# Performance work log

Measured on AMD Instinct MI355X. Metric: run time of the kernel, lower is better.

The kernel has to match this reference:

```python
import jax, jax.numpy as jnp
import numpy as np

NUM_HEADS = 16

def _rope_tables(seq_len, head_dim, dtype):
    inv_freq = 1.0 / (10000.0 ** (jnp.arange(0, head_dim, 2, dtype=jnp.float32) / head_dim))
    t = jnp.arange(seq_len, dtype=jnp.float32)
    freqs = jnp.einsum('i,j->ij', t, inv_freq)          # [S, hd/2]
    emb = jnp.concatenate([freqs, freqs], axis=-1)      # [S, hd]
    return jnp.cos(emb).astype(dtype), jnp.sin(emb).astype(dtype)

def _rotate_half(x):
    x1, x2 = jnp.split(x, 2, axis=-1)
    return jnp.concatenate([-x2, x1], axis=-1)

def _apply_rope(x, cos, sin):
    # x: [B, H, S, hd]; cos/sin: [S, hd]
    return x * cos + _rotate_half(x) * sin

def setup_inputs() -> dict:
    key = jax.random.key(0)
    ks = jax.random.split(key, 9)
    S, B, E = 2048, 2, 1024
    sc_w = 1.0 / np.sqrt(E)
    inp = {
        'query': jax.random.normal(ks[0], (S, B, E), jnp.float32),
        'wq': jax.random.normal(ks[1], (E, E), jnp.float32) * sc_w,
        'bq': jax.random.normal(ks[2], (E,), jnp.float32) * 0.02,
        'wk': jax.random.normal(ks[3], (E, E), jnp.float32) * sc_w,
        'bk': jax.random.normal(ks[4], (E,), jnp.float32) * 0.02,
        'wv': jax.random.normal(ks[5], (E, E), jnp.float32) * sc_w,
        'bv': jax.random.normal(ks[6], (E,), jnp.float32) * 0.02,
        'wo': jax.random.normal(ks[7], (E, E), jnp.float32) * sc_w,
        'bo': jax.random.normal(ks[8], (E,), jnp.float32) * 0.02,
    }
    return inp

def reference(query, wq, bq, wk, bk, wv, bv, wo, bo):
    S, B, E = query.shape
    H = NUM_HEADS
    hd = E // H
    # QKV projections (torch Linear: x @ W^T + b). self_attention => k,v from query.
    q = jnp.einsum('sbe,fe->sbf', query, wq) + bq
    k = jnp.einsum('sbe,fe->sbf', query, wk) + bk
    v = jnp.einsum('sbe,fe->sbf', query, wv) + bv
    # [S, B, E] -> [B, H, S, hd]
    def to_bhsd(x):
        return x.reshape(S, B, H, hd).transpose(1, 2, 0, 3)
    q, k, v = to_bhsd(q), to_bhsd(k), to_bhsd(v)
    cos, sin = _rope_tables(S, hd, query.dtype)
    q = _apply_rope(q, cos, sin)
    k = _apply_rope(k, cos, sin)
    # scaled dot-product attention (no mask, no dropout)
    scale = 1.0 / jnp.sqrt(jnp.asarray(hd, query.dtype))
    scores = jnp.einsum('bhqd,bhkd->bhqk', q, k) * scale
    probs = jax.nn.softmax(scores, axis=-1)
    attn = jnp.einsum('bhqk,bhkd->bhqd', probs, v)
    # [B, H, S, hd] -> [S, B, E]
    attn = attn.transpose(2, 0, 1, 3).reshape(S, B, E)
    out = jnp.einsum('sbe,fe->sbf', attn, wo) + bo
    return out
```

## Files before the change

### kernel.cpp

```cpp
#include <hip/hip_runtime.h>
#include <stdint.h>

#define S_LEN 2048
#define BATCH 2
#define EMB   1024
#define NHEAD 16
#define HDIM  64

typedef __bf16 bf8   __attribute__((ext_vector_type(8)));
typedef float  f32x4 __attribute__((ext_vector_type(4)));
typedef float  f32x16 __attribute__((ext_vector_type(16)));

__device__ __forceinline__ unsigned short f2bf(float f) {
    unsigned u = __builtin_bit_cast(unsigned, f);
    u += 0x7fffu + ((u >> 16) & 1u);
    return (unsigned short)(u >> 16);
}
__device__ __forceinline__ float bf2f(unsigned short h) {
    unsigned u = ((unsigned)h) << 16;
    return __builtin_bit_cast(float, u);
}
__device__ __forceinline__ float fexp2(float x) { return __builtin_amdgcn_exp2f(x); }
__device__ __forceinline__ float f3max(float a, float b, float c) { return fmaxf(fmaxf(a, b), c); }

__device__ __forceinline__ void gl_lds16(const unsigned short* g, unsigned short* l) {
    __builtin_amdgcn_global_load_lds(
        (__attribute__((address_space(1))) void*)(void*)g,
        (__attribute__((address_space(3))) void*)(void*)l, 16, 0, 0);
}

__global__ void k_tables(float* __restrict__ cosT, float* __restrict__ sinT) {
    int idx = blockIdx.x * 256 + threadIdx.x;
    int s = idx >> 6, d = idx & 63, j = d & 31;
    float inv = exp2f(-13.28771237954945f * ((float)j * (1.0f / 32.0f)));
    float ang = (float)s * inv;
    cosT[idx] = cosf(ang);
    sinT[idx] = sinf(ang);
}

__global__ void k_cast_x(const float* __restrict__ x, unsigned short* __restrict__ xb) {
    int id = blockIdx.x * 256 + threadIdx.x;
    int b = id >> 19, rem = id & 524287;
    int s = rem >> 8, e4 = (rem & 255) << 2;
    float4 v = *(const float4*)&x[((size_t)(s * BATCH + b)) * EMB + e4];
    ushort4 o;
    o.x = f2bf(v.x); o.y = f2bf(v.y); o.z = f2bf(v.z); o.w = f2bf(v.w);
    *(ushort4*)&xb[((size_t)(b * S_LEN + s)) * EMB + e4] = o;
}

__global__ void k_castW(const float* __restrict__ w0, const float* __restrict__ w1,
                        const float* __restrict__ w2, const float* __restrict__ w3,
                        unsigned short* __restrict__ o0, unsigned short* __restrict__ o1,
                        unsigned short* __restrict__ o2, unsigned short* __restrict__ o3) {
    int id = blockIdx.x * 256 + threadIdx.x;
    int seg = id >> 18, r = id & 262143;
    const float* s = seg == 0 ? w0 : seg == 1 ? w1 : seg == 2 ? w2 : w3;
    unsigned short* o = seg == 0 ? o0 : seg == 1 ? o1 : seg == 2 ? o2 : o3;
    float4 v = *(const float4*)&s[(size_t)r * 4];
    ushort4 u;
    u.x = f2bf(v.x); u.y = f2bf(v.y); u.z = f2bf(v.z); u.w = f2bf(v.w);
    *(ushort4*)&o[(size_t)r * 4] = u;
}

__global__ void __launch_bounds__(256) k_gemmQKV(
    const unsigned short* __restrict__ A,
    const unsigned short* __restrict__ Wq, const unsigned short* __restrict__ Wk,
    const unsigned short* __restrict__ Wv,
    const float* __restrict__ bqp, const float* __restrict__ bkp, const float* __restrict__ bvp,
    unsigned short* __restrict__ qout, unsigned short* __restrict__ kout,
    unsigned short* __restrict__ vout,
    const float* __restrict__ cosT, const float* __restrict__ sinT)
{
    __shared__ __align__(16) unsigned short As[128 * 32];
    __shared__ __align__(16) unsigned short Bs[128 * 32];
    const int z = blockIdx.z;
    const unsigned short* B = z == 0 ? Wq : z == 1 ? Wk : Wv;
    const float* bias = z == 0 ? bqp : z == 1 ? bkp : bvp;
    const int tid  = threadIdx.x;
    const int lane = tid & 63;
    const int wid  = tid >> 6;
    const int wm = wid >> 1, wn = wid & 1;
    const int l15 = lane & 15, lh = lane >> 4;
    const int tm0 = blockIdx.y * 128, tn0 = blockIdx.x * 128;
    const int K = 1024;

    f32x4 acc[4][4] = {};

    for (int k0 = 0; k0 < K; k0 += 32) {
        __syncthreads();
#pragma unroll
        for (int rnd = 0; rnd < 2; ++rnd) {
            int cbase = wid * 64 + rnd * 256;
            int c = cbase + lane;
            int row = c >> 2, co = (c & 3) * 8;
            gl_lds16(A + (size_t)(tm0 + row) * K + k0 + co, &As[cbase * 8]);
            gl_lds16(B + (size_t)(tn0 + row) * K + k0 + co, &Bs[cbase * 8]);
        }
        __syncthreads();
        bf8 a[4], b[4];
#pragma unroll
        for (int i = 0; i < 4; ++i) {
            a[i] = *(const bf8*)&As[(wm * 64 + i * 16 + l15) * 32 + lh * 8];
            b[i] = *(const bf8*)&Bs[(wn * 64 + i * 16 + l15) * 32 + lh * 8];
        }
#pragma unroll
        for (int i = 0; i < 4; ++i)
#pragma unroll
            for (int j = 0; j < 4; ++j)
                acc[i][j] = __builtin_amdgcn_mfma_f32_16x16x32_bf16(a[i], b[j], acc[i][j], 0, 0, 0);
    }

    if (z < 2) {
        unsigned short* C = z ? kout : qout;
        const float f = z ? 1.0f : 0.125f * 1.44269504089f;
#pragma unroll
        for (int i = 0; i < 4; ++i) {
            const int rowb = tm0 + wm * 64 + i * 16 + lh * 4;
#pragma unroll
            for (int j = 0; j < 2; ++j) {
                const int col = tn0 + wn * 64 + j * 16 + l15;
                const int d = j * 16 + l15;
#pragma unroll
                for (int r = 0; r < 4; ++r) {
                    int m = rowb + r;
                    int sq = m & (S_LEN - 1);
                    float x1 = acc[i][j][r]     + bias[col];
                    float x2 = acc[i][j + 2][r] + bias[col + 32];
                    float c  = cosT[sq * 64 + d] * f;
                    float sn = sinT[sq * 64 + d] * f;
                    C[(size_t)m * EMB + col]      = f2bf(x1 * c - x2 * sn);
                    C[(size_t)m * EMB + col + 32] = f2bf(x2 * c + x1 * sn);
                }
            }
        }
    } else {
#pragma unroll
        for (int i = 0; i < 4; ++i) {
            const int rowb = tm0 + wm * 64 + i * 16 + lh * 4;
#pragma unroll
            for (int j = 0; j < 4; ++j) {
                const int col = tn0 + wn * 64 + j * 16 + l15;
                float bv = bias[col];
#pragma unroll
                for (int r = 0; r < 4; ++r)
                    vout[(size_t)col * 4096 + rowb + r] = f2bf(acc[i][j][r] + bv);
            }
        }
    }
}

__global__ void __launch_bounds__(256) k_attn8(
    const unsigned short* __restrict__ qb,
    const unsigned short* __restrict__ kb,
    const unsigned short* __restrict__ vT,
    float* __restrict__ po0, float* __restrict__ po1,
    float* __restrict__ ml)
{
    __shared__ __align__(16) unsigned short Sm[24576];
    __shared__ float bl[4][32];
    const int tid = threadIdx.x, lane = tid & 63, wid = tid >> 6;
    const int l31 = lane & 31, hi = lane >> 5;
    const int bh = blockIdx.y;
    const int b = bh >> 4, h = bh & 15;
    const int z = blockIdx.z;
    const int kv0 = z << 10;
    const int q0 = blockIdx.x * 128 + wid * 32;
    float* __restrict__ po = z ? po1 : po0;
    float* __restrict__ mlz = ml + (size_t)z * (32 * 2048 * 2);

    const unsigned short* qrow = qb + ((size_t)(b * S_LEN + q0 + l31)) * EMB + h * HDIM + hi * 8;
    bf8 qf[4];
#pragma unroll
    for (int c = 0; c < 4; ++c) qf[c] = *(const bf8*)(qrow + c * 16);

    const int mz = l31 & 7;
    const int koA0 = l31 * 128 + (((0 * 2 + hi) ^ mz) << 4);
    const int koA1 = l31 * 128 + (((1 * 2 + hi) ^ mz) << 4);
    const int koA2 = l31 * 128 + (((2 * 2 + hi) ^ mz) << 4);
    const int koA3 = l31 * 128 + (((3 * 2 + hi) ^ mz) << 4);
    const char* ldsc = (const char*)Sm;

    const int srow = lane >> 3, sp = lane & 7;
    const int r0 = wid * 16 + srow,     p0s = sp ^ (r0 & 7);
    const int r1 = wid * 16 + 8 + srow, p1s = sp ^ (r1 & 7);
    const int kgo0 = (r0 * EMB + p0s * 8) * 2, kgo1 = (r1 * EMB + p1s * 8) * 2;
    const int vgo0 = (r0 * (S_LEN * BATCH) + p0s * 8) * 2, vgo1 = (r1 * (S_LEN * BATCH) + p1s * 8) * 2;

    const unsigned short* kS = kb + ((size_t)(b * S_LEN + kv0)) * EMB + h * HDIM;
    const unsigned short* vS = vT + ((size_t)h * HDIM) * (S_LEN * BATCH) + b * S_LEN + kv0;

#define STAGE8(DBUF) do { \
    gl_lds16((const unsigned short*)((const char*)kS + kgo0), Sm + (DBUF) * 4096 + wid * 1024); \
    gl_lds16((const unsigned short*)((const char*)vS + vgo0), Sm + 12288 + (DBUF) * 4096 + wid * 1024); \
    gl_lds16((const unsigned short*)((const char*)kS + kgo1), Sm + (DBUF) * 4096 + wid * 1024 + 512); \
    gl_lds16((const unsigned short*)((const char*)vS + vgo1), Sm + 12288 + (DBUF) * 4096 + wid * 1024 + 512); \
    kS += 64 * EMB; vS += 64; } while (0)

    auto pack2 = [](float lo, float hh) -> unsigned {
        unsigned short a  = __builtin_bit_cast(unsigned short, (__bf16)lo);
        unsigned short bb = __builtin_bit_cast(unsigned short, (__bf16)hh);
        return ((unsigned)bb << 16) | a;
    };

    float m_run = 0.f, l_run = 0.f;
    f32x16 oacc0 = {}, oacc1 = {};
    const f32x16 Z16 = {};

    STAGE8(0);
    STAGE8(1);

#define ABODY(BUF, DOSTG, LASTW) do { \
    if (LASTW) asm volatile("s_waitcnt vmcnt(0)" ::: "memory"); \
    else       asm volatile("s_waitcnt vmcnt(4)" ::: "memory"); \
    __builtin_amdgcn_s_barrier(); \
    if (DOSTG) STAGE8(((BUF) + 2) % 3); \
    bf8 ka0 = *(const bf8*)(ldsc + koA0 + (BUF) * 8192); \
    bf8 ka1 = *(const bf8*)(ldsc + koA1 + (BUF) * 8192); \
    bf8 ka2 = *(const bf8*)(ldsc + koA2 + (BUF) * 8192); \
    bf8 ka3 = *(const bf8*)(ldsc + koA3 + (BUF) * 8192); \
    bf8 kb0 = *(const bf8*)(ldsc + koA0 + (BUF) * 8192 + 4096); \
    bf8 kb1 = *(const bf8*)(ldsc + koA1 + (BUF) * 8192 + 4096); \
    bf8 kb2 = *(const bf8*)(ldsc + koA2 + (BUF) * 8192 + 4096); \
    bf8 kb3 = *(const bf8*)(ldsc + koA3 + (BUF) * 8192 + 4096); \
    __builtin_amdgcn_s_setprio(1); \
    f32x16 stA = __builtin_amdgcn_mfma_f32_32x32x16_bf16(ka0, qf[0], Z16, 0, 0, 0); \
    f32x16 stB = __builtin_amdgcn_mfma_f32_32x32x16_bf16(kb0, qf[0], Z16, 0, 0, 0); \
    stA = __builtin_amdgcn_mfma_f32_32x32x16_bf16(ka1, qf[1], stA, 0, 0, 0); \
    stB = __builtin_amdgcn_mfma_f32_32x32x16_bf16(kb1, qf[1], stB, 0, 0, 0); \
    stA = __builtin_amdgcn_mfma_f32_32x32x16_bf16(ka2, qf[2], stA, 0, 0, 0); \
    stB = __builtin_amdgcn_mfma_f32_32x32x16_bf16(kb2, qf[2], stB, 0, 0, 0); \
    stA = __builtin_amdgcn_mfma_f32_32x32x16_bf16(ka3, qf[3], stA, 0, 0, 0); \
    stB = __builtin_amdgcn_mfma_f32_32x32x16_bf16(kb3, qf[3], stB, 0, 0, 0); \
    __builtin_amdgcn_s_setprio(0); \
    float g0 = f3max(f3max(stA[0], stA[1], stA[2]),  f3max(stA[3], stA[4], stA[5]),  f3max(stA[6], stA[7], stA[8])); \
    float g1 = f3max(f3max(stA[9], stA[10], stA[11]), f3max(stA[12], stA[13], stA[14]), fmaxf(stA[15], stB[0])); \
    float g2 = f3max(f3max(stB[1], stB[2], stB[3]),  f3max(stB[4], stB[5], stB[6]),  f3max(stB[7], stB[8], stB[9])); \
    float g3 = f3max(f3max(stB[10], stB[11], stB[12]), f3max(stB[13], stB[14], stB[15]), fmaxf(g0, g1)); \
    float pmax = f3max(g2, g3, g0); \
    pmax = fmaxf(pmax, __shfl_xor(pmax, 32)); \
    if (!__all(pmax - m_run <= 11.54f)) { \
        float mnew = fmaxf(m_run, pmax); \
        float corr = fexp2(m_run - mnew); \
        l_run *= corr; m_run = mnew; \
        if (hi == 0) bl[wid][l31] = corr; \
        asm volatile("s_waitcnt lgkmcnt(0)" ::: "memory"); \
        _Pragma("unroll") for (int r = 0; r < 16; ++r) { \
            float c2 = bl[wid][(r & 3) + 8 * (r >> 2) + 4 * hi]; \
            oacc0[r] *= c2; oacc1[r] *= c2; } \
    } \
    float pA[16], pB[16]; \
    _Pragma("unroll") for (int r = 0; r < 16; ++r) pA[r] = fexp2(stA[r] - m_run); \
    _Pragma("unroll") for (int r = 0; r < 16; ++r) pB[r] = fexp2(stB[r] - m_run); \
    float sA = (((pA[0] + pA[1]) + (pA[2] + pA[3])) + ((pA[4] + pA[5]) + (pA[6] + pA[7]))) \
             + (((pA[8] + pA[9]) + (pA[10] + pA[11])) + ((pA[12] + pA[13]) + (pA[14] + pA[15]))); \
    float sB = (((pB[0] + pB[1]) + (pB[2] + pB[3])) + ((pB[4] + pB[5]) + (pB[6] + pB[7]))) \
             + (((pB[8] + pB[9]) + (pB[10] + pB[11])) + ((pB[12] + pB[13]) + (pB[14] + pB[15]))); \
    float psum = sA + sB; \
    psum += __shfl_xor(psum, 32); \
    l_run += psum; \
    unsigned a0w = pack2(pA[0], pA[1]),  a1w = pack2(pA[2], pA[3]); \
    unsigned a2w = pack2(pA[4], pA[5]),  a3w = pack2(pA[6], pA[7]); \
    unsigned a4w = pack2(pA[8], pA[9]),  a5w = pack2(pA[10], pA[11]); \
    unsigned a6w = pack2(pA[12], pA[13]), a7w = pack2(pA[14], pA[15]); \
    unsigned rA_ = (unsigned)__shfl_xor((int)(hi ? a0w : a2w), 32); \
    unsigned rB_ = (unsigned)__shfl_xor((int)(hi ? a1w : a3w), 32); \
    unsigned rC_ = (unsigned)__shfl_xor((int)(hi ? a4w : a6w), 32); \
    unsigned rD_ = (unsigned)__shfl_xor((int)(hi ? a5w : a7w), 32); \
    uint4 uA0 = hi ? uint4{rA_, rB_, a2w, a3w} : uint4{a0w, a1w, rA_, rB_}; \
    uint4 uA1 = hi ? uint4{rC_, rD_, a6w, a7w} : uint4{a4w, a5w, rC_, rD_}; \
    bf8 pf0A = __builtin_bit_cast(bf8, uA0); \
    bf8 pf1A = __builtin_bit_cast(bf8, uA1); \
    unsigned b0w = pack2(pB[0], pB[1]),  b1w = pack2(pB[2], pB[3]); \
    unsigned b2w = pack2(pB[4], pB[5]),  b3w = pack2(pB[6], pB[7]); \
    unsigned b4w = pack2(pB[8], pB[9]),  b5w = pack2(pB[10], pB[11]); \
    unsigned b6w = pack2(pB[12], pB[13]), b7w = pack2(pB[14], pB[15]); \
    unsigned rE_ = (unsigned)__shfl_xor((int)(hi ? b0w : b2w), 32); \
    unsigned rF_ = (unsigned)__shfl_xor((int)(hi ? b1w : b3w), 32); \
    unsigned rG_ = (unsigned)__shfl_xor((int)(hi ? b4w : b6w), 32); \
    unsigned rH_ = (unsigned)__shfl_xor((int)(hi ? b5w : b7w), 32); \
    uint4 uB0 = hi ? uint4{rE_, rF_, b2w, b3w} : uint4{b0w, b1w, rE_, rF_}; \
    uint4 uB1 = hi ? uint4{rG_, rH_, b6w, b7w} : uint4{b4w, b5w, rG_, rH_}; \
    bf8 pf0B = __builtin_bit_cast(bf8, uB0); \
    bf8 pf1B = __builtin_bit_cast(bf8, uB1); \
    bf8 va0 = *(const bf8*)(ldsc + koA0 + 24576 + (BUF) * 8192); \
    bf8 va1 = *(const bf8*)(ldsc + koA1 + 24576 + (BUF) * 8192); \
    bf8 va2 = *(const bf8*)(ldsc + koA2 + 24576 + (BUF) * 8192); \
    bf8 va3 = *(const bf8*)(ldsc + koA3 + 24576 + (BUF) * 8192); \
    bf8 vb0 = *(const bf8*)(ldsc + koA0 + 24576 + (BUF) * 8192 + 4096); \
    bf8 vb1 = *(const bf8*)(ldsc + koA1 + 24576 + (BUF) * 8192 + 4096); \
    bf8 vb2 = *(const bf8*)(ldsc + koA2 + 24576 + (BUF) * 8192 + 4096); \
    bf8 vb3 = *(const bf8*)(ldsc + koA3 + 24576 + (BUF) * 8192 + 4096); \
    __builtin_amdgcn_s_setprio(1); \
    oacc0 = __builtin_amdgcn_mfma_f32_32x32x16_bf16(pf0A, va0, oacc0, 0, 0, 0); \
    oacc1 = __builtin_amdgcn_mfma_f32_32x32x16_bf16(pf0A, vb0, oacc1, 0, 0, 0); \
    oacc0 = __builtin_amdgcn_mfma_f32_32x32x16_bf16(pf1A, va1, oacc0, 0, 0, 0); \
    oacc1 = __builtin_amdgcn_mfma_f32_32x32x16_bf16(pf1A, vb1, oacc1, 0, 0, 0); \
    oacc0 = __builtin_amdgcn_mfma_f32_32x32x16_bf16(pf0B, va2, oacc0, 0, 0, 0); \
    oacc1 = __builtin_amdgcn_mfma_f32_32x32x16_bf16(pf0B, vb2, oacc1, 0, 0, 0); \
    oacc0 = __builtin_amdgcn_mfma_f32_32x32x16_bf16(pf1B, va3, oacc0, 0, 0, 0); \
    oacc1 = __builtin_amdgcn_mfma_f32_32x32x16_bf16(pf1B, vb3, oacc1, 0, 0, 0); \
    __builtin_amdgcn_s_setprio(0); \
} while (0)

    for (int t3 = 0; t3 < 5; ++t3) {
        ABODY(0, true, false);
        ABODY(1, true, false);
        ABODY(2, (t3 < 4), false);
    }
    ABODY(0, false, true);

#undef ABODY
#undef STAGE8

#pragma unroll
    for (int r = 0; r < 16; ++r) {
        int q = (r & 3) + 8 * (r >> 2) + 4 * hi;
        size_t base = ((size_t)bh * 2048 + q0 + q) * 64 + l31;
        po[base]      = oacc0[r];
        po[base + 32] = oacc1[r];
    }
    if (hi == 0) {
        size_t mi = ((size_t)bh * 2048 + q0 + l31) * 2;
        mlz[mi]     = m_run;
        mlz[mi + 1] = l_run;
    }
}

__global__ void k_comb(const float* __restrict__ po0, const float* __restrict__ po1,
                       const float* __restrict__ ml, unsigned short* __restrict__ ob)
{
    int id = blockIdx.x * 256 + threadIdx.x;
    int d4 = (id & 15) * 4;
    int q  = (id >> 4) & 2047;
    int bh = id >> 15;
    int b = bh >> 4, h = bh & 15;
    size_t mi = ((size_t)bh * 2048 + q) * 2;
    float m0 = ml[mi], l0 = ml[mi + 1];
    float m1 = ml[mi + (size_t)32 * 2048 * 2], l1 = ml[mi + (size_t)32 * 2048 * 2 + 1];
    float m = fmaxf(m0, m1);
    float w0 = fexp2(m0 - m), w1 = fexp2(m1 - m);
    float inv = 1.0f / (l0 * w0 + l1 * w1);
    size_t pi = ((size_t)bh * 2048 + q) * 64 + d4;
    float4 a = *(const float4*)&po0[pi];
    float4 c = *(const float4*)&po1[pi];
    ushort4 o;
    o.x = f2bf((a.x * w0 + c.x * w1) * inv);
    o.y = f2bf((a.y * w0 + c.y * w1) * inv);
    o.z = f2bf((a.z * w0 + c.z * w1) * inv);
    o.w = f2bf((a.w * w0 + c.w * w1) * inv);
    *(ushort4*)&ob[((size_t)(b * S_LEN + q)) * EMB + h * HDIM + d4] = o;
}

template<int EPI, typename OutT>
__global__ void __launch_bounds__(256) k_gemm(
    const unsigned short* __restrict__ A,
    const unsigned short* __restrict__ B,
    const float* __restrict__ bias,
    OutT* __restrict__ C,
    int M, int N, int K)
{
    __shared__ __align__(16) unsigned short As[128 * 32];
    __shared__ __align__(16) unsigned short Bs[128 * 32];
    const int tid  = threadIdx.x;
    const int lane = tid & 63;
    const int wid  = tid >> 6;
    const int wm = wid >> 1, wn = wid & 1;
    const int l15 = lane & 15, lh = lane >> 4;
    const int tm0 = blockIdx.y * 128, tn0 = blockIdx.x * 128;

    f32x4 acc[4][4] = {};

    for (int k0 = 0; k0 < K; k0 += 32) {
        __syncthreads();
#pragma unroll
        for (int rnd = 0; rnd < 2; ++rnd) {
            int cbase = wid * 64 + rnd * 256;
            int c = cbase + lane;
            int row = c >> 2, co = (c & 3) * 8;
            gl_lds16(A + (size_t)(tm0 + row) * K + k0 + co, &As[cbase * 8]);
            gl_lds16(B + (size_t)(tn0 + row) * K + k0 + co, &Bs[cbase * 8]);
        }
        __syncthreads();
        bf8 a[4], b[4];
#pragma unroll
        for (int i = 0; i < 4; ++i) {
            a[i] = *(const bf8*)&As[(wm * 64 + i * 16 + l15) * 32 + lh * 8];
            b[i] = *(const bf8*)&Bs[(wn * 64 + i * 16 + l15) * 32 + lh * 8];
        }
#pragma unroll
        for (int i = 0; i < 4; ++i)
#pragma unroll
            for (int j = 0; j < 4; ++j)
                acc[i][j] = __builtin_amdgcn_mfma_f32_16x16x32_bf16(a[i], b[j], acc[i][j], 0, 0, 0);
    }

#pragma unroll
    for (int i = 0; i < 4; ++i) {
        const int rowb = tm0 + wm * 64 + i * 16 + lh * 4;
#pragma unroll
        for (int j = 0; j < 4; ++j) {
            const int col = tn0 + wn * 64 + j * 16 + l15;
#pragma unroll
            for (int r = 0; r < 4; ++r) {
                float v = acc[i][j][r];
                int row = rowb + r;
                if (EPI == 0) {
                    v += bias[col];
                    C[(size_t)row * N + col] = (OutT)f2bf(v);
                } else {
                    v += bias[col];
                    int bb = row >> 11, ss = row & 2047;
                    ((float*)C)[(size_t)(ss * BATCH + bb) * N + col] = v;
                }
            }
        }
    }
}

extern "C" void kernel_launch(void* const* d_in, const int* in_sizes, int n_in,
                              void* d_out, int out_size, void* d_ws, size_t ws_size,
                              hipStream_t stream)
{
    (void)in_sizes; (void)n_in; (void)out_size; (void)ws_size;
    const float* query = (const float*)d_in[0];
    const float* wq = (const float*)d_in[1];
    const float* bq = (const float*)d_in[2];
    const float* wk = (const float*)d_in[3];
    const float* bk = (const float*)d_in[4];
    const float* wv = (const float*)d_in[5];
    const float* bv = (const float*)d_in[6];
    const float* wo = (const float*)d_in[7];
    const float* bo = (const float*)d_in[8];

    char* ws = (char*)d_ws;
    float*          cosT = (float*)(ws + 0);
    float*          sinT = (float*)(ws + (512 << 10));
    float*          ml   = (float*)(ws + 0);
    unsigned short* xb   = (unsigned short*)(ws + (1  << 20));
    float*          po0  = (float*)(ws + (1  << 20));
    unsigned short* wqb  = (unsigned short*)(ws + (9  << 20));
    unsigned short* wkb  = (unsigned short*)(ws + (11 << 20));
    unsigned short* wvb  = (unsigned short*)(ws + (13 << 20));
    unsigned short* qb   = (unsigned short*)(ws + (17 << 20));
    unsigned short* ob   = qb;
    unsigned short* kb   = (unsigned short*)(ws + (25 << 20));
    unsigned short* vT   = (unsigned short*)(ws + (33 << 20));
    float*          po1  = (float*)(ws + (41 << 20));
    unsigned short* wob  = (unsigned short*)(ws + (57 << 20));

    k_tables<<<512, 256, 0, stream>>>(cosT, sinT);
    k_cast_x<<<4096, 256, 0, stream>>>(query, xb);
    k_castW<<<4096, 256, 0, stream>>>(wq, wk, wv, wo, wqb, wkb, wvb, wob);

    dim3 gq(EMB / 128, (S_LEN * BATCH) / 128, 3);
    k_gemmQKV<<<gq, 256, 0, stream>>>(xb, wqb, wkb, wvb, bq, bk, bv,
                                      qb, kb, vT, cosT, sinT);

    dim3 g3(S_LEN / 128, BATCH * NHEAD, 2);
    k_attn8<<<g3, 256, 0, stream>>>(qb, kb, vT, po0, po1, ml);
    k_comb<<<4096, 256, 0, stream>>>(po0, po1, ml, ob);

    dim3 g1(EMB / 128, (S_LEN * BATCH) / 128);
    k_gemm<1, float><<<g1, 256, 0, stream>>>(ob, wob, bo, (float*)d_out, 4096, 1024, 1024);
}
```

Baseline: 168.0 us.

## Drop split-KV attention and fuse the three prep kernels into one launch

The attention kernel now sweeps the full KV length in one block instead of two KV halves. It normalizes by the running sum in its epilogue and writes bf16 output directly, so the fp32 partial buffers and the separate combine kernel go away. The table, activation-cast and weight-cast kernels are merged into a single launch that dispatches on block index. This saves launches and the partial-output traffic, but halves the attention grid, which lowers parallelism (512 blocks instead of 1024) and doubles each block's serial loop length.

```diff
diff --git a/kernel.cpp b/kernel.cpp
--- a/kernel.cpp
+++ b/kernel.cpp
@@ -29,37 +29,40 @@
         (__attribute__((address_space(3))) void*)(void*)l, 16, 0, 0);
 }
 
-__global__ void k_tables(float* __restrict__ cosT, float* __restrict__ sinT) {
-    int idx = blockIdx.x * 256 + threadIdx.x;
-    int s = idx >> 6, d = idx & 63, j = d & 31;
-    float inv = exp2f(-13.28771237954945f * ((float)j * (1.0f / 32.0f)));
-    float ang = (float)s * inv;
-    cosT[idx] = cosf(ang);
-    sinT[idx] = sinf(ang);
-}
-
-__global__ void k_cast_x(const float* __restrict__ x, unsigned short* __restrict__ xb) {
-    int id = blockIdx.x * 256 + threadIdx.x;
-    int b = id >> 19, rem = id & 524287;
-    int s = rem >> 8, e4 = (rem & 255) << 2;
-    float4 v = *(const float4*)&x[((size_t)(s * BATCH + b)) * EMB + e4];
-    ushort4 o;
-    o.x = f2bf(v.x); o.y = f2bf(v.y); o.z = f2bf(v.z); o.w = f2bf(v.w);
-    *(ushort4*)&xb[((size_t)(b * S_LEN + s)) * EMB + e4] = o;
-}
-
-__global__ void k_castW(const float* __restrict__ w0, const float* __restrict__ w1,
-                        const float* __restrict__ w2, const float* __restrict__ w3,
-                        unsigned short* __restrict__ o0, unsigned short* __restrict__ o1,
-                        unsigned short* __restrict__ o2, unsigned short* __restrict__ o3) {
-    int id = blockIdx.x * 256 + threadIdx.x;
-    int seg = id >> 18, r = id & 262143;
-    const float* s = seg == 0 ? w0 : seg == 1 ? w1 : seg == 2 ? w2 : w3;
-    unsigned short* o = seg == 0 ? o0 : seg == 1 ? o1 : seg == 2 ? o2 : o3;
-    float4 v = *(const float4*)&s[(size_t)r * 4];
-    ushort4 u;
-    u.x = f2bf(v.x); u.y = f2bf(v.y); u.z = f2bf(v.z); u.w = f2bf(v.w);
-    *(ushort4*)&o[(size_t)r * 4] = u;
+__global__ void k_prep(const float* __restrict__ x,
+                       const float* __restrict__ w0, const float* __restrict__ w1,
+                       const float* __restrict__ w2, const float* __restrict__ w3,
+                       float* __restrict__ cosT, float* __restrict__ sinT,
+                       unsigned short* __restrict__ xb,
+                       unsigned short* __restrict__ o0, unsigned short* __restrict__ o1,
+                       unsigned short* __restrict__ o2, unsigned short* __restrict__ o3)
+{
+    int bid = blockIdx.x;
+    if (bid < 512) {
+        int idx = bid * 256 + threadIdx.x;
+        int s = idx >> 6, d = idx & 63, j = d & 31;
+        float inv = exp2f(-13.28771237954945f * ((float)j * (1.0f / 32.0f)));
+        float ang = (float)s * inv;
+        cosT[idx] = cosf(ang);
+        sinT[idx] = sinf(ang);
+    } else if (bid < 4608) {
+        int id = (bid - 512) * 256 + threadIdx.x;
+        int b = id >> 19, rem = id & 524287;
+        int s = rem >> 8, e4 = (rem & 255) << 2;
+        float4 v = *(const float4*)&x[((size_t)(s * BATCH + b)) * EMB + e4];
+        ushort4 o;
+        o.x = f2bf(v.x); o.y = f2bf(v.y); o.z = f2bf(v.z); o.w = f2bf(v.w);
+        *(ushort4*)&xb[((size_t)(b * S_LEN + s)) * EMB + e4] = o;
+    } else {
+        int id = (bid - 4608) * 256 + threadIdx.x;
+        int seg = id >> 18, r = id & 262143;
+        const float* s = seg == 0 ? w0 : seg == 1 ? w1 : seg == 2 ? w2 : w3;
+        unsigned short* o = seg == 0 ? o0 : seg == 1 ? o1 : seg == 2 ? o2 : o3;
+        float4 v = *(const float4*)&s[(size_t)r * 4];
+        ushort4 u;
+        u.x = f2bf(v.x); u.y = f2bf(v.y); u.z = f2bf(v.z); u.w = f2bf(v.w);
+        *(ushort4*)&o[(size_t)r * 4] = u;
+    }
 }
 
 __global__ void __launch_bounds__(256) k_gemmQKV(
@@ -153,8 +156,7 @@
     const unsigned short* __restrict__ qb,
     const unsigned short* __restrict__ kb,
     const unsigned short* __restrict__ vT,
-    float* __restrict__ po0, float* __restrict__ po1,
-    float* __restrict__ ml)
+    unsigned short* __restrict__ ob)
 {
     __shared__ __align__(16) unsigned short Sm[24576];
     __shared__ float bl[4][32];
@@ -162,11 +164,7 @@
     const int l31 = lane & 31, hi = lane >> 5;
     const int bh = blockIdx.y;
     const int b = bh >> 4, h = bh & 15;
-    const int z = blockIdx.z;
-    const int kv0 = z << 10;
     const int q0 = blockIdx.x * 128 + wid * 32;
-    float* __restrict__ po = z ? po1 : po0;
-    float* __restrict__ mlz = ml + (size_t)z * (32 * 2048 * 2);
 
     const unsigned short* qrow = qb + ((size_t)(b * S_LEN + q0 + l31)) * EMB + h * HDIM + hi * 8;
     bf8 qf[4];
@@ -186,8 +184,8 @@
     const int kgo0 = (r0 * EMB + p0s * 8) * 2, kgo1 = (r1 * EMB + p1s * 8) * 2;
     const int vgo0 = (r0 * (S_LEN * BATCH) + p0s * 8) * 2, vgo1 = (r1 * (S_LEN * BATCH) + p1s * 8) * 2;
 
-    const unsigned short* kS = kb + ((size_t)(b * S_LEN + kv0)) * EMB + h * HDIM;
-    const unsigned short* vS = vT + ((size_t)h * HDIM) * (S_LEN * BATCH) + b * S_LEN + kv0;
+    const unsigned short* kS = kb + ((size_t)(b * S_LEN)) * EMB + h * HDIM;
+    const unsigned short* vS = vT + ((size_t)h * HDIM) * (S_LEN * BATCH) + b * S_LEN;
 
 #define STAGE8(DBUF) do { \
     gl_lds16((const unsigned short*)((const char*)kS + kgo0), Sm + (DBUF) * 4096 + wid * 1024); \
@@ -302,53 +300,27 @@
     __builtin_amdgcn_s_setprio(0); \
 } while (0)
 
-    for (int t3 = 0; t3 < 5; ++t3) {
+    for (int t3 = 0; t3 < 10; ++t3) {
         ABODY(0, true, false);
         ABODY(1, true, false);
-        ABODY(2, (t3 < 4), false);
-    }
-    ABODY(0, false, true);
+        ABODY(2, true, false);
+    }
+    ABODY(0, false, false);
+    ABODY(1, false, true);
 
 #undef ABODY
 #undef STAGE8
 
+    if (hi == 0) bl[wid][l31] = l_run;
+    asm volatile("s_waitcnt lgkmcnt(0)" ::: "memory");
 #pragma unroll
     for (int r = 0; r < 16; ++r) {
         int q = (r & 3) + 8 * (r >> 2) + 4 * hi;
-        size_t base = ((size_t)bh * 2048 + q0 + q) * 64 + l31;
-        po[base]      = oacc0[r];
-        po[base + 32] = oacc1[r];
-    }
-    if (hi == 0) {
-        size_t mi = ((size_t)bh * 2048 + q0 + l31) * 2;
-        mlz[mi]     = m_run;
-        mlz[mi + 1] = l_run;
-    }
-}
-
-__global__ void k_comb(const float* __restrict__ po0, const float* __restrict__ po1,
-                       const float* __restrict__ ml, unsigned short* __restrict__ ob)
-{
-    int id = blockIdx.x * 256 + threadIdx.x;
-    int d4 = (id & 15) * 4;
-    int q  = (id >> 4) & 2047;
-    int bh = id >> 15;
-    int b = bh >> 4, h = bh & 15;
-    size_t mi = ((size_t)bh * 2048 + q) * 2;
-    float m0 = ml[mi], l0 = ml[mi + 1];
-    float m1 = ml[mi + (size_t)32 * 2048 * 2], l1 = ml[mi + (size_t)32 * 2048 * 2 + 1];
-    float m = fmaxf(m0, m1);
-    float w0 = fexp2(m0 - m), w1 = fexp2(m1 - m);
-    float inv = 1.0f / (l0 * w0 + l1 * w1);
-    size_t pi = ((size_t)bh * 2048 + q) * 64 + d4;
-    float4 a = *(const float4*)&po0[pi];
-    float4 c = *(const float4*)&po1[pi];
-    ushort4 o;
-    o.x = f2bf((a.x * w0 + c.x * w1) * inv);
-    o.y = f2bf((a.y * w0 + c.y * w1) * inv);
-    o.z = f2bf((a.z * w0 + c.z * w1) * inv);
-    o.w = f2bf((a.w * w0 + c.w * w1) * inv);
-    *(ushort4*)&ob[((size_t)(b * S_LEN + q)) * EMB + h * HDIM + d4] = o;
+        float linv = 1.0f / bl[wid][q];
+        size_t base = ((size_t)(b * S_LEN + q0 + q)) * EMB + h * HDIM + l31;
+        ob[base]      = f2bf(oacc0[r] * linv);
+        ob[base + 32] = f2bf(oacc1[r] * linv);
+    }
 }
 
 template<int EPI, typename OutT>
@@ -435,30 +407,25 @@
     char* ws = (char*)d_ws;
     float*          cosT = (float*)(ws + 0);
     float*          sinT = (float*)(ws + (512 << 10));
-    float*          ml   = (float*)(ws + 0);
     unsigned short* xb   = (unsigned short*)(ws + (1  << 20));
-    float*          po0  = (float*)(ws + (1  << 20));
     unsigned short* wqb  = (unsigned short*)(ws + (9  << 20));
     unsigned short* wkb  = (unsigned short*)(ws + (11 << 20));
     unsigned short* wvb  = (unsigned short*)(ws + (13 << 20));
+    unsigned short* wob  = (unsigned short*)(ws + (15 << 20));
     unsigned short* qb   = (unsigned short*)(ws + (17 << 20));
     unsigned short* ob   = qb;
     unsigned short* kb   = (unsigned short*)(ws + (25 << 20));
     unsigned short* vT   = (unsigned short*)(ws + (33 << 20));
-    float*          po1  = (float*)(ws + (41 << 20));
-    unsigned short* wob  = (unsigned short*)(ws + (57 << 20));
-
-    k_tables<<<512, 256, 0, stream>>>(cosT, sinT);
-    k_cast_x<<<4096, 256, 0, stream>>>(query, xb);
-    k_castW<<<4096, 256, 0, stream>>>(wq, wk, wv, wo, wqb, wkb, wvb, wob);
+
+    k_prep<<<8704, 256, 0, stream>>>(query, wq, wk, wv, wo,
+                                     cosT, sinT, xb, wqb, wkb, wvb, wob);
 
     dim3 gq(EMB / 128, (S_LEN * BATCH) / 128, 3);
     k_gemmQKV<<<gq, 256, 0, stream>>>(xb, wqb, wkb, wvb, bq, bk, bv,
                                       qb, kb, vT, cosT, sinT);
 
-    dim3 g3(S_LEN / 128, BATCH * NHEAD, 2);
-    k_attn8<<<g3, 256, 0, stream>>>(qb, kb, vT, po0, po1, ml);
-    k_comb<<<4096, 256, 0, stream>>>(po0, po1, ml, ob);
+    dim3 g3(S_LEN / 128, BATCH * NHEAD);
+    k_attn8<<<g3, 256, 0, stream>>>(qb, kb, vT, ob);
 
     dim3 g1(EMB / 128, (S_LEN * BATCH) / 128);
     k_gemm<1, float><<<g1, 256, 0, stream>>>(ob, wob, bo, (float*)d_out, 4096, 1024, 1024);
```

New measurement: 153.8 us. -8.4%, faster.
